# Kernel tuning notes

Measured on AMD Instinct MI355X. Metric: run time of the kernel, lower is better.

Reference implementation:

```python
import jax, jax.numpy as jnp
import numpy as np

NODE, PROJ, ATTN, NREL, NL = 1280, 2560, 256, 129, 4
B, L = 2, 1024
EPS = 1e-5


def _layernorm(x):
    m = jnp.mean(x, axis=-1, keepdims=True)
    v = jnp.var(x, axis=-1, keepdims=True)
    return (x - m) * jax.lax.rsqrt(v + EPS)


def _rope(x):
    # x: [B, L, 2, D]; rotary applied along the seq (L) axis, rotate-half convention
    d = x.shape[-1]
    freq = 10000.0 ** (-jnp.arange(0, d, 2, dtype=jnp.float32) / d)      # [d/2]
    ang = jnp.arange(x.shape[1], dtype=jnp.float32)[:, None] * freq      # [L, d/2]
    cos = jnp.concatenate([jnp.cos(ang), jnp.cos(ang)], -1)[:, None, :]  # [L,1,d]
    sin = jnp.concatenate([jnp.sin(ang), jnp.sin(ang)], -1)[:, None, :]
    x1, x2 = jnp.split(x, 2, axis=-1)
    return x * cos + jnp.concatenate([-x2, x1], -1) * sin


def _relpos_idx(n):
    i = np.arange(n)
    one = NREL // 2
    return jnp.asarray(np.clip(i[:, None] - i[None, :], -one, one) + one)  # [L,L] int32


def setup_inputs() -> dict:
    key = jax.random.key(0)
    ks = jax.random.split(key, 14)
    s = 0.02
    return {
        "node": jax.random.normal(ks[0], (B, L, NODE), jnp.float32),
        "qk_scaling": jax.random.uniform(ks[1], (B, L, 1), jnp.float32),
        "bias": jax.random.normal(ks[2], (B, 1, L), jnp.float32),
        "cond": jax.random.normal(ks[3], (B, NODE), jnp.float32),
        "w_gva": jax.random.normal(ks[4], (NL, NODE, 2 * PROJ + ATTN), jnp.float32) * s,
        "b_gva": jnp.zeros((NL, 2 * PROJ + ATTN), jnp.float32),
        "mhs_w": jax.random.normal(ks[5], (NL, 2, ATTN), jnp.float32) * s + 1.0,
        "mhs_b": jax.random.normal(ks[6], (NL, 2, ATTN), jnp.float32) * s,
        "relpos_emb": jax.random.normal(ks[7], (NL, NREL), jnp.float32) * s,
        "w_out": jax.random.normal(ks[8], (NL, PROJ, NODE), jnp.float32) * s,
        "b_out": jnp.zeros((NL, NODE), jnp.float32),
        "w_adaln": jax.random.normal(ks[9], (NL, NODE, 3 * NODE), jnp.float32) * s,
        "b_adaln": jnp.zeros((NL, 3 * NODE), jnp.float32),
        "subbatch_size": 256,
    }


def _forward(node, qk_scaling, bias, cond, w_gva, b_gva, mhs_w, mhs_b,
             relpos_emb, w_out, b_out, w_adaln, b_adaln, rel_idx):
    edge = None
    silu = jax.nn.silu
    for l in range(NL):
        # AdaLN conditioning: SiLU -> Linear(node, 3*node), chunk into gamma/beta/alpha [B,node]
        gba = silu(cond) @ w_adaln[l] + b_adaln[l]
        gamma, beta, alpha = jnp.split(gba, 3, axis=-1)
        shortcut = node
        x = _layernorm(node)
        x = x * (1.0 + gamma[:, None, :]) + beta[:, None, :]
        # GAU: joint gate/value/base projection + SiLU
        h = silu(x @ w_gva[l] + b_gva[l])                    # [B,L,2P+A]
        gates = h[..., :PROJ]
        values = h[..., PROJ:2 * PROJ]
        base = h[..., 2 * PROJ:]                             # [B,L,A]
        # multi-headed scaling (2 heads) + RoPE, unbind into q,k
        qk = base[..., None, :] * mhs_w[l] + mhs_b[l]        # [B,L,2,A]
        qk = _rope(qk)
        q, k = qk[..., 0, :], qk[..., 1, :]
        # attention with mask bias + relpos bias; query pre-scaled
        rel = relpos_emb[l][rel_idx]                         # [L,L]
        logits = jnp.einsum('bid,bjd->bij', q * qk_scaling, k) + (bias + rel)
        attn = jax.nn.softmax(logits, axis=-1)               # [B,L,L]
        out = jnp.einsum('bij,bjd->bid', attn, values)       # [B,L,P]
        edge = jnp.sum(attn, axis=-3)                        # sum-reduce over batch -> [L,L]
        out = out * gates
        out = out @ w_out[l] + b_out[l]
        node = out * (1.0 + alpha[:, None, :]) + shortcut
    return node, edge


def reference(node, qk_scaling, bias, cond, w_gva, b_gva, mhs_w, mhs_b,
              relpos_emb, w_out, b_out, w_adaln, b_adaln, subbatch_size):
    # subbatch_size only chunks queries for memory in the original; math-identical ignored
    rel_idx = _relpos_idx(node.shape[-2])
    return _forward(node, qk_scaling, bias, cond, w_gva, b_gva, mhs_w, mhs_b,
                    relpos_emb, w_out, b_out, w_adaln, b_adaln, rel_idx)
```

## Files before the change

kernel.cpp:

```cpp
#include <hip/hip_runtime.h>


typedef __bf16 bf16;
typedef __attribute__((ext_vector_type(8))) __bf16 bf16x8;
typedef __attribute__((ext_vector_type(4))) float f32x4;

#define NODE_D 1280
#define PROJ_D 2560
#define ATTN_D 256
#define HDIM 5376
#define LSEQ 1024
#define NTOK 2048

__device__ __forceinline__ void async_ld16(const void* gsrc, void* ldst) {
  __builtin_amdgcn_global_load_lds(
      (__attribute__((address_space(1))) void*)gsrc,
      (__attribute__((address_space(3))) void*)ldst, 16, 0, 0);
}

__device__ __forceinline__ float sigmoidf_fast(float x) {
  return 1.f / (1.f + __expf(-x));
}

template <int MODE>
__global__ __launch_bounds__(256, 3) void gemm_bt(
    const bf16* __restrict__ A, const bf16* __restrict__ Bt, int K,
    int lda, int ldb, void* __restrict__ C, int ldc,
    const void* __restrict__ E0, const void* __restrict__ E1,
    long zA, long zB, long zCb, long zE0b) {
  __shared__ __align__(16) bf16 As[128 * 32];
  __shared__ __align__(16) bf16 Bs[128 * 32];

  const int z = blockIdx.z;
  A += (size_t)zA * z;
  Bt += (size_t)zB * z;
  char* Cb = (char*)C + (size_t)zCb * z;
  const char* e0 = (const char*)E0 + (size_t)zE0b * z;

  const int rowBase = blockIdx.y * 128;
  const int colBase = blockIdx.x * 128;
  const int tid = threadIdx.x;
  const int lane = tid & 63;
  const int wv = tid >> 6;
  const int srow = lane >> 2;
  const int scol = (lane & 3) * 8;
  const int wrow = (wv >> 1) * 64;
  const int wcol = (wv & 1) * 64;
  const int fm = lane & 15;
  const int fq = lane >> 4;

  const bf16* Ablk = A + (size_t)rowBase * lda;
  const bf16* Bblk = Bt + (size_t)colBase * ldb;

  f32x4 zero = {0.f, 0.f, 0.f, 0.f};
  f32x4 acc[4][4];
#pragma unroll
  for (int i = 0; i < 4; i++)
#pragma unroll
    for (int j = 0; j < 4; j++) acc[i][j] = zero;

  for (int k0 = 0; k0 < K; k0 += 32) {
    __syncthreads();
#pragma unroll
    for (int i = 0; i < 2; i++) {
      const int c = wv * 2 + i;
      async_ld16(Ablk + (size_t)(c * 16 + srow) * lda + k0 + scol, As + c * 512);
      async_ld16(Bblk + (size_t)(c * 16 + srow) * ldb + k0 + scol, Bs + c * 512);
    }
    __syncthreads();

    bf16x8 aF[4], bF[4];
#pragma unroll
    for (int i = 0; i < 4; i++)
      aF[i] = *(const bf16x8*)(As + (wrow + i * 16 + fm) * 32 + fq * 8);
#pragma unroll
    for (int j = 0; j < 4; j++)
      bF[j] = *(const bf16x8*)(Bs + (wcol + j * 16 + fm) * 32 + fq * 8);
#pragma unroll
    for (int i = 0; i < 4; i++)
#pragma unroll
      for (int j = 0; j < 4; j++)
        acc[i][j] = __builtin_amdgcn_mfma_f32_16x16x32_bf16(aF[i], bF[j],
                                                            acc[i][j], 0, 0, 0);
  }

#pragma unroll
  for (int i = 0; i < 4; i++) {
#pragma unroll
    for (int t = 0; t < 4; t++) {
      const int r = rowBase + wrow + i * 16 + fq * 4 + t;
#pragma unroll
      for (int j = 0; j < 4; j++) {
        const int cc = colBase + wcol + j * 16 + fm;
        float v = acc[i][j][t];
        if constexpr (MODE == 0) {
          v += ((const float*)e0)[cc];
          v = v * sigmoidf_fast(v);
          ((bf16*)Cb)[(size_t)r * ldc + cc] = (bf16)v;
        } else if constexpr (MODE == 1) {
          v += ((const float*)e0)[cc];
          int d = r - cc;
          d = d < -64 ? -64 : (d > 64 ? 64 : d);
          v += ((const float*)E1)[d + 64];
          ((float*)Cb)[(size_t)r * ldc + cc] = v;
        } else if constexpr (MODE == 2) {
          float gt = (float)((const bf16*)e0)[(size_t)r * HDIM + cc];
          ((bf16*)Cb)[(size_t)r * ldc + cc] = (bf16)(v * gt);
        } else {
          ((float*)Cb)[(size_t)r * ldc + cc] = v;
        }
      }
    }
  }
}

__global__ void transpose_f2b(const float* __restrict__ in, bf16* __restrict__ out,
                              int ldin, int ldout) {
  __shared__ __align__(16) bf16 t[64][72];
  const int rb = blockIdx.y * 64, cb = blockIdx.x * 64;
  const int tx = threadIdx.x & 7, ty = threadIdx.x >> 3;
#pragma unroll
  for (int rr = 0; rr < 64; rr += 32) {
    const int r = ty + rr;
    const float4* p = (const float4*)&in[(size_t)(rb + r) * ldin + cb + tx * 8];
    float4 a = p[0], b = p[1];
    t[tx * 8 + 0][r] = (bf16)a.x; t[tx * 8 + 1][r] = (bf16)a.y;
    t[tx * 8 + 2][r] = (bf16)a.z; t[tx * 8 + 3][r] = (bf16)a.w;
    t[tx * 8 + 4][r] = (bf16)b.x; t[tx * 8 + 5][r] = (bf16)b.y;
    t[tx * 8 + 6][r] = (bf16)b.z; t[tx * 8 + 7][r] = (bf16)b.w;
  }
  __syncthreads();
#pragma unroll
  for (int rr = 0; rr < 64; rr += 32) {
    const int c = ty + rr;
    *(bf16x8*)&out[(size_t)(cb + c) * ldout + rb + tx * 8] =
        *(const bf16x8*)&t[c][tx * 8];
  }
}

__global__ void transpose_int(const bf16* __restrict__ in0, bf16* __restrict__ out0,
                              int ldin, int ldout, long zIn, long zOut) {
  __shared__ __align__(16) bf16 t[64][72];
  const bf16* in = in0 + (size_t)zIn * blockIdx.z;
  bf16* out = out0 + (size_t)zOut * blockIdx.z;
  const int rb = blockIdx.y * 64, cb = blockIdx.x * 64;
  const int tx = threadIdx.x & 7, ty = threadIdx.x >> 3;
#pragma unroll
  for (int rr = 0; rr < 64; rr += 32) {
    const int r = ty + rr;
    bf16x8 v = *(const bf16x8*)&in[(size_t)(rb + r) * ldin + cb + tx * 8];
#pragma unroll
    for (int e = 0; e < 8; e++) t[tx * 8 + e][r] = v[e];
  }
  __syncthreads();
#pragma unroll
  for (int rr = 0; rr < 64; rr += 32) {
    const int c = ty + rr;
    *(bf16x8*)&out[(size_t)(cb + c) * ldout + rb + tx * 8] =
        *(const bf16x8*)&t[c][tx * 8];
  }
}

__global__ void gba_init(const float* __restrict__ b_adaln,
                         float* __restrict__ gba) {
  const int i = blockIdx.x * 256 + threadIdx.x;
  if (i < 4 * 2 * 3840) {
    const int l = i / (2 * 3840);
    const int c = i % 3840;
    gba[i] = b_adaln[l * 3840 + c];
  }
}

__global__ void adaln_part(const float* __restrict__ cond,
                           const float* __restrict__ w_adaln,
                           float* __restrict__ gba) {
  __shared__ float sc[2 * NODE_D];
  __shared__ float red[2][2][128];
  const int l = blockIdx.y, z = blockIdx.z;
  const int cl = threadIdx.x & 127;
  const int col = blockIdx.x * 128 + cl;
  const int kg = threadIdx.x >> 7;
  for (int i = threadIdx.x; i < 2 * NODE_D; i += 256) {
    float v = cond[i];
    sc[i] = v * sigmoidf_fast(v);
  }
  __syncthreads();
  const float* w = w_adaln + (size_t)l * NODE_D * 3840;
  const int k0 = z * 160 + kg * 80;
  float a0 = 0.f, a1 = 0.f;
  for (int k = k0; k < k0 + 80; k++) {
    float wv = w[(size_t)k * 3840 + col];
    a0 += sc[k] * wv;
    a1 += sc[NODE_D + k] * wv;
  }
  red[kg][0][cl] = a0;
  red[kg][1][cl] = a1;
  __syncthreads();
  if (kg == 0) {
    a0 += red[1][0][cl];
    a1 += red[1][1][cl];
    atomicAdd(&gba[(size_t)(l * 2 + 0) * 3840 + col], a0);
    atomicAdd(&gba[(size_t)(l * 2 + 1) * 3840 + col], a1);
  }
}

__global__ void ln_mod_kernel(const float* __restrict__ nodef,
                              const float* __restrict__ gba_l,
                              bf16* __restrict__ xmod) {
  __shared__ float red[2][4];
  const int row = blockIdx.x, b = row >> 10, tt = threadIdx.x;
  const float* x = nodef + (size_t)row * NODE_D;
  float vals[5], s = 0.f, s2 = 0.f;
#pragma unroll
  for (int i = 0; i < 5; i++) {
    float v = x[tt + i * 256];
    vals[i] = v; s += v; s2 += v * v;
  }
#pragma unroll
  for (int off = 32; off >= 1; off >>= 1) {
    s += __shfl_down(s, off, 64);
    s2 += __shfl_down(s2, off, 64);
  }
  const int wv = tt >> 6, lane = tt & 63;
  if (lane == 0) { red[0][wv] = s; red[1][wv] = s2; }
  __syncthreads();
  s = red[0][0] + red[0][1] + red[0][2] + red[0][3];
  s2 = red[1][0] + red[1][1] + red[1][2] + red[1][3];
  const float mean = s * (1.f / NODE_D);
  const float var = s2 * (1.f / NODE_D) - mean * mean;
  const float inv = rsqrtf(var + 1e-5f);
  const float* gm = gba_l + b * 3840;
#pragma unroll
  for (int i = 0; i < 5; i++) {
    const int c = tt + i * 256;
    float v = (vals[i] - mean) * inv * (1.f + gm[c]) + gm[NODE_D + c];
    xmod[(size_t)row * NODE_D + c] = (bf16)v;
  }
}

template <bool LAST>
__global__ void res_ln_fuse(const float* __restrict__ p0,
                            const float* __restrict__ p1,
                            const float* __restrict__ b_out_l,
                            const float* __restrict__ gba_l,
                            const float* __restrict__ gba_next,
                            float* __restrict__ nodef,
                            bf16* __restrict__ xmod,
                            float* __restrict__ outNode) {
  __shared__ float red[2][4];
  const int row = blockIdx.x, b = row >> 10, tt = threadIdx.x;
  const float* a0 = p0 + (size_t)row * NODE_D;
  const float* a1 = p1 + (size_t)row * NODE_D;
  float* nd = nodef + (size_t)row * NODE_D;
  const float* al = gba_l + b * 3840 + 2560;
  float vals[5], s = 0.f, s2 = 0.f;
#pragma unroll
  for (int i = 0; i < 5; i++) {
    const int c = tt + i * 256;
    float delta = (a0[c] + a1[c] + b_out_l[c]) * (1.f + al[c]);
    float v = nd[c] + delta;
    if (LAST) {
      outNode[(size_t)row * NODE_D + c] = v;
    } else {
      nd[c] = v;
    }
    vals[i] = v; s += v; s2 += v * v;
  }
  if (!LAST) {
#pragma unroll
    for (int off = 32; off >= 1; off >>= 1) {
      s += __shfl_down(s, off, 64);
      s2 += __shfl_down(s2, off, 64);
    }
    const int wv = tt >> 6, lane = tt & 63;
    if (lane == 0) { red[0][wv] = s; red[1][wv] = s2; }
    __syncthreads();
    s = red[0][0] + red[0][1] + red[0][2] + red[0][3];
    s2 = red[1][0] + red[1][1] + red[1][2] + red[1][3];
    const float mean = s * (1.f / NODE_D);
    const float var = s2 * (1.f / NODE_D) - mean * mean;
    const float inv = rsqrtf(var + 1e-5f);
    const float* gm = gba_next + b * 3840;
#pragma unroll
    for (int i = 0; i < 5; i++) {
      const int c = tt + i * 256;
      float v = (vals[i] - mean) * inv * (1.f + gm[c]) + gm[NODE_D + c];
      xmod[(size_t)row * NODE_D + c] = (bf16)v;
    }
  }
}

__global__ void qk_rope_kernel(const bf16* __restrict__ h,
                               const float* __restrict__ mhs_w,
                               const float* __restrict__ mhs_b,
                               const float* __restrict__ qk_sc,
                               bf16* __restrict__ q, bf16* __restrict__ k) {
  const int tok = blockIdx.x;
  const int pos = tok & (LSEQ - 1);
  const int d = threadIdx.x;
  const bf16* base = h + (size_t)tok * HDIM + 2 * PROJ_D;
  const int j = d & 127;
  const float freq = __expf(-(float)j * 0.07195578415606392f);
  const float ang = (float)pos * freq;
  const float cs = cosf(ang), sn = sinf(ang);
  const float bd = (float)base[d];
  const int pd = (d < 128) ? d + 128 : d - 128;
  const float bp = (float)base[pd];
  const float sgn = (d < 128) ? -1.f : 1.f;

  float v = bd * mhs_w[d] + mhs_b[d];
  float vp = bp * mhs_w[pd] + mhs_b[pd];
  float r0 = v * cs + sgn * vp * sn;
  q[(size_t)tok * ATTN_D + d] = (bf16)(r0 * qk_sc[tok]);

  float v1 = bd * mhs_w[ATTN_D + d] + mhs_b[ATTN_D + d];
  float v1p = bp * mhs_w[ATTN_D + pd] + mhs_b[ATTN_D + pd];
  float r1 = v1 * cs + sgn * v1p * sn;
  k[(size_t)tok * ATTN_D + d] = (bf16)r1;
}

__global__ void softmax_kernel(const float* __restrict__ S, bf16* __restrict__ P) {
  __shared__ float red[8];
  const size_t row = blockIdx.x;
  const float* s = S + row * LSEQ;
  const int tt = threadIdx.x, wv = tt >> 6, lane = tt & 63;
  float v[4];
  float m = -1e30f;
#pragma unroll
  for (int i = 0; i < 4; i++) {
    v[i] = s[tt + i * 256];
    m = fmaxf(m, v[i]);
  }
#pragma unroll
  for (int off = 32; off >= 1; off >>= 1) m = fmaxf(m, __shfl_down(m, off, 64));
  if (lane == 0) red[wv] = m;
  __syncthreads();
  m = fmaxf(fmaxf(red[0], red[1]), fmaxf(red[2], red[3]));
  float sum = 0.f;
#pragma unroll
  for (int i = 0; i < 4; i++) {
    v[i] = __expf(v[i] - m);
    sum += v[i];
  }
#pragma unroll
  for (int off = 32; off >= 1; off >>= 1) sum += __shfl_down(sum, off, 64);
  __syncthreads();
  if (lane == 0) red[4 + wv] = sum;
  __syncthreads();
  const float inv = 1.f / (red[4] + red[5] + red[6] + red[7]);
  bf16* p = P + row * LSEQ;
#pragma unroll
  for (int i = 0; i < 4; i++) p[tt + i * 256] = (bf16)(v[i] * inv);
}

__global__ void copy_f32(const float* __restrict__ in, float* __restrict__ out,
                         int n) {
  int i = (blockIdx.x * 256 + threadIdx.x) * 4;
  if (i < n) *(float4*)(out + i) = *(const float4*)(in + i);
}

__global__ void edge_kernel(const bf16* __restrict__ P, float* __restrict__ out) {
  const int idx = (blockIdx.x * 256 + threadIdx.x) * 4;
#pragma unroll
  for (int i = 0; i < 4; i++)
    out[idx + i] = (float)P[idx + i] + (float)P[1048576 + idx + i];
}

extern "C" void kernel_launch(void* const* d_in, const int* in_sizes, int n_in,
                              void* d_out, int out_size, void* d_ws, size_t ws_size,
                              hipStream_t stream) {
  const float* node_in = (const float*)d_in[0];
  const float* qk_sc   = (const float*)d_in[1];
  const float* bias    = (const float*)d_in[2];
  const float* cond    = (const float*)d_in[3];
  const float* w_gva   = (const float*)d_in[4];
  const float* b_gva   = (const float*)d_in[5];
  const float* mhs_w   = (const float*)d_in[6];
  const float* mhs_b   = (const float*)d_in[7];
  const float* relpos  = (const float*)d_in[8];
  const float* w_out   = (const float*)d_in[9];
  const float* b_out   = (const float*)d_in[10];
  const float* w_adaln = (const float*)d_in[11];
  const float* b_adaln = (const float*)d_in[12];
  (void)in_sizes; (void)n_in; (void)out_size; (void)ws_size;

  char* wsp = (char*)d_ws;
  auto alloc = [&](size_t bytes) {
    char* p = wsp;
    wsp += (bytes + 255) & ~(size_t)255;
    return p;
  };
  float* nodef = (float*)alloc((size_t)NTOK * NODE_D * 4);
  float* gba   = (float*)alloc((size_t)8 * 3840 * 4);
  bf16* xmod   = (bf16*)alloc((size_t)NTOK * NODE_D * 2);
  bf16* h      = (bf16*)alloc((size_t)NTOK * HDIM * 2);
  bf16* q      = (bf16*)alloc((size_t)NTOK * ATTN_D * 2);
  bf16* kk     = (bf16*)alloc((size_t)NTOK * ATTN_D * 2);
  bf16* Vt     = (bf16*)alloc((size_t)2 * PROJ_D * LSEQ * 2);
  bf16* wT     = (bf16*)alloc((size_t)HDIM * NODE_D * 2);
  float* S     = (float*)wT;
  bf16* P      = (bf16*)alloc((size_t)2 * LSEQ * LSEQ * 2);
  bf16* po     = (bf16*)alloc((size_t)NTOK * PROJ_D * 2);
  float* Pp    = (float*)alloc((size_t)2 * NTOK * NODE_D * 4);

  float* outNode = (float*)d_out;
  float* outEdge = outNode + (size_t)NTOK * NODE_D;

  copy_f32<<<2560, 256, 0, stream>>>(node_in, nodef, NTOK * NODE_D);
  gba_init<<<120, 256, 0, stream>>>(b_adaln, gba);
  adaln_part<<<dim3(30, 4, 8), 256, 0, stream>>>(cond, w_adaln, gba);
  ln_mod_kernel<<<2048, 256, 0, stream>>>(nodef, gba, xmod);

  for (int l = 0; l < 4; ++l) {
    transpose_f2b<<<dim3(84, 20), 256, 0, stream>>>(
        w_gva + (size_t)l * NODE_D * HDIM, wT, HDIM, NODE_D);
    gemm_bt<0><<<dim3(42, 16, 1), 256, 0, stream>>>(
        xmod, wT, NODE_D, NODE_D, NODE_D, h, HDIM,
        b_gva + (size_t)l * HDIM, nullptr, 0, 0, 0, 0);

    qk_rope_kernel<<<2048, 256, 0, stream>>>(h, mhs_w + l * 2 * ATTN_D,
                                             mhs_b + l * 2 * ATTN_D, qk_sc, q, kk);

    transpose_int<<<dim3(40, 16, 2), 256, 0, stream>>>(
        h + PROJ_D, Vt, HDIM, LSEQ, (long)LSEQ * HDIM, (long)PROJ_D * LSEQ);

    gemm_bt<1><<<dim3(8, 8, 2), 256, 0, stream>>>(
        q, kk, ATTN_D, ATTN_D, ATTN_D, S, LSEQ,
        bias, relpos + l * 129,
        (long)LSEQ * ATTN_D, (long)LSEQ * ATTN_D, (long)LSEQ * LSEQ * 4,
        (long)LSEQ * 4);

    softmax_kernel<<<2048, 256, 0, stream>>>(S, P);
    if (l == 3) edge_kernel<<<1024, 256, 0, stream>>>(P, outEdge);

    gemm_bt<2><<<dim3(20, 8, 2), 256, 0, stream>>>(
        P, Vt, LSEQ, LSEQ, LSEQ, po, PROJ_D,
        h, nullptr,
        (long)LSEQ * LSEQ, (long)PROJ_D * LSEQ, (long)LSEQ * PROJ_D * 2,
        (long)LSEQ * HDIM * 2);

    transpose_f2b<<<dim3(20, 40), 256, 0, stream>>>(
        w_out + (size_t)l * PROJ_D * NODE_D, wT, NODE_D, PROJ_D);
    gemm_bt<4><<<dim3(10, 16, 2), 256, 0, stream>>>(
        po, wT, 1280, PROJ_D, PROJ_D, Pp, NODE_D,
        nullptr, nullptr,
        1280, 1280, (long)NTOK * NODE_D * 4, 0);

    if (l < 3) {
      res_ln_fuse<false><<<2048, 256, 0, stream>>>(
          Pp, Pp + (size_t)NTOK * NODE_D, b_out + (size_t)l * NODE_D,
          gba + l * 2 * 3840, gba + (l + 1) * 2 * 3840, nodef, xmod, nullptr);
    } else {
      res_ln_fuse<true><<<2048, 256, 0, stream>>>(
          Pp, Pp + (size_t)NTOK * NODE_D, b_out + (size_t)l * NODE_D,
          gba + l * 2 * 3840, nullptr, nodef, nullptr, outNode);
    }
  }
}
```

Before: 872.4 us.

## Double GEMM K-tile to 64 with XOR-swizzled LDS and precompute RoPE trig table

The shared GEMM kernel now stages 64-wide K slices instead of 32, halving the number of barrier pairs per K loop. Shared memory rows are XOR-swizzled so the wider rows do not cause LDS bank conflicts on fragment reads. Separately, the RoPE cos/sin values are computed once into a table by a new init kernel, replacing per-layer transcendental calls in qk_rope. The larger LDS footprint (32 KB per block) may reduce occupancy under the launch_bounds of 3 blocks.

```diff
diff --git a/kernel.cpp b/kernel.cpp
--- a/kernel.cpp
+++ b/kernel.cpp
@@ -28,8 +28,8 @@
     int lda, int ldb, void* __restrict__ C, int ldc,
     const void* __restrict__ E0, const void* __restrict__ E1,
     long zA, long zB, long zCb, long zE0b) {
-  __shared__ __align__(16) bf16 As[128 * 32];
-  __shared__ __align__(16) bf16 Bs[128 * 32];
+  __shared__ __align__(16) bf16 As[128 * 64];
+  __shared__ __align__(16) bf16 Bs[128 * 64];
 
   const int z = blockIdx.z;
   A += (size_t)zA * z;
@@ -42,8 +42,6 @@
   const int tid = threadIdx.x;
   const int lane = tid & 63;
   const int wv = tid >> 6;
-  const int srow = lane >> 2;
-  const int scol = (lane & 3) * 8;
   const int wrow = (wv >> 1) * 64;
   const int wcol = (wv & 1) * 64;
   const int fm = lane & 15;
@@ -59,29 +57,42 @@
 #pragma unroll
     for (int j = 0; j < 4; j++) acc[i][j] = zero;
 
-  for (int k0 = 0; k0 < K; k0 += 32) {
+  for (int k0 = 0; k0 < K; k0 += 64) {
     __syncthreads();
 #pragma unroll
-    for (int i = 0; i < 2; i++) {
-      const int c = wv * 2 + i;
-      async_ld16(Ablk + (size_t)(c * 16 + srow) * lda + k0 + scol, As + c * 512);
-      async_ld16(Bblk + (size_t)(c * 16 + srow) * ldb + k0 + scol, Bs + c * 512);
+    for (int i = 0; i < 4; i++) {
+      const int slot = tid + i * 256;
+      const int row = slot >> 3;
+      const int u = (slot & 7) ^ (row & 7);
+      bf16* dA = As + ((i * 256 + wv * 64) << 3);
+      bf16* dB = Bs + ((i * 256 + wv * 64) << 3);
+      async_ld16(Ablk + (size_t)row * lda + k0 + (u << 3), dA);
+      async_ld16(Bblk + (size_t)row * ldb + k0 + (u << 3), dB);
     }
     __syncthreads();
 
-    bf16x8 aF[4], bF[4];
-#pragma unroll
-    for (int i = 0; i < 4; i++)
-      aF[i] = *(const bf16x8*)(As + (wrow + i * 16 + fm) * 32 + fq * 8);
-#pragma unroll
-    for (int j = 0; j < 4; j++)
-      bF[j] = *(const bf16x8*)(Bs + (wcol + j * 16 + fm) * 32 + fq * 8);
-#pragma unroll
-    for (int i = 0; i < 4; i++)
-#pragma unroll
-      for (int j = 0; j < 4; j++)
-        acc[i][j] = __builtin_amdgcn_mfma_f32_16x16x32_bf16(aF[i], bF[j],
-                                                            acc[i][j], 0, 0, 0);
+#pragma unroll
+    for (int s = 0; s < 2; s++) {
+      bf16x8 aF[4], bF[4];
+#pragma unroll
+      for (int i = 0; i < 4; i++) {
+        const int r = wrow + i * 16 + fm;
+        aF[i] = *(const bf16x8*)(As + r * 64 +
+                                 ((((s << 2) | fq) ^ (r & 7)) << 3));
+      }
+#pragma unroll
+      for (int j = 0; j < 4; j++) {
+        const int r = wcol + j * 16 + fm;
+        bF[j] = *(const bf16x8*)(Bs + r * 64 +
+                                 ((((s << 2) | fq) ^ (r & 7)) << 3));
+      }
+#pragma unroll
+      for (int i = 0; i < 4; i++)
+#pragma unroll
+        for (int j = 0; j < 4; j++)
+          acc[i][j] = __builtin_amdgcn_mfma_f32_16x16x32_bf16(
+              aF[i], bF[j], acc[i][j], 0, 0, 0);
+    }
   }
 
 #pragma unroll
@@ -290,19 +301,28 @@
   }
 }
 
+__global__ void trig_init(float* __restrict__ tab) {
+  const int pos = blockIdx.x;
+  const int j = threadIdx.x;
+  const float freq = __expf(-(float)j * 0.07195578415606392f);
+  const float ang = (float)pos * freq;
+  tab[(pos * 128 + j) * 2 + 0] = cosf(ang);
+  tab[(pos * 128 + j) * 2 + 1] = sinf(ang);
+}
+
 __global__ void qk_rope_kernel(const bf16* __restrict__ h,
                                const float* __restrict__ mhs_w,
                                const float* __restrict__ mhs_b,
                                const float* __restrict__ qk_sc,
+                               const float* __restrict__ trig,
                                bf16* __restrict__ q, bf16* __restrict__ k) {
   const int tok = blockIdx.x;
   const int pos = tok & (LSEQ - 1);
   const int d = threadIdx.x;
   const bf16* base = h + (size_t)tok * HDIM + 2 * PROJ_D;
   const int j = d & 127;
-  const float freq = __expf(-(float)j * 0.07195578415606392f);
-  const float ang = (float)pos * freq;
-  const float cs = cosf(ang), sn = sinf(ang);
+  const float2 cssn = ((const float2*)trig)[pos * 128 + j];
+  const float cs = cssn.x, sn = cssn.y;
   const float bd = (float)base[d];
   const int pd = (d < 128) ? d + 128 : d - 128;
   const float bp = (float)base[pd];
@@ -402,11 +422,13 @@
   bf16* P      = (bf16*)alloc((size_t)2 * LSEQ * LSEQ * 2);
   bf16* po     = (bf16*)alloc((size_t)NTOK * PROJ_D * 2);
   float* Pp    = (float*)alloc((size_t)2 * NTOK * NODE_D * 4);
+  float* trig  = (float*)alloc((size_t)LSEQ * 128 * 2 * 4);
 
   float* outNode = (float*)d_out;
   float* outEdge = outNode + (size_t)NTOK * NODE_D;
 
   copy_f32<<<2560, 256, 0, stream>>>(node_in, nodef, NTOK * NODE_D);
+  trig_init<<<1024, 128, 0, stream>>>(trig);
   gba_init<<<120, 256, 0, stream>>>(b_adaln, gba);
   adaln_part<<<dim3(30, 4, 8), 256, 0, stream>>>(cond, w_adaln, gba);
   ln_mod_kernel<<<2048, 256, 0, stream>>>(nodef, gba, xmod);
@@ -419,7 +441,8 @@
         b_gva + (size_t)l * HDIM, nullptr, 0, 0, 0, 0);
 
     qk_rope_kernel<<<2048, 256, 0, stream>>>(h, mhs_w + l * 2 * ATTN_D,
-                                             mhs_b + l * 2 * ATTN_D, qk_sc, q, kk);
+                                             mhs_b + l * 2 * ATTN_D, qk_sc,
+                                             trig, q, kk);
 
     transpose_int<<<dim3(40, 16, 2), 256, 0, stream>>>(
         h + PROJ_D, Vt, HDIM, LSEQ, (long)LSEQ * HDIM, (long)PROJ_D * LSEQ);
```

Measured after the change: 793.6 us. 9.0% less time.
